# Optimization experiments

Measured on AMD Instinct MI355X. Metric: run time of the kernel, lower is better.

## Reference

```python
import jax, jax.numpy as jnp
import numpy as np

B_SZ = 64
SEQ = 2048
IN_DIM = 16
D_MODEL = 128
D_INNER = 256   # expand(2) * d_model
D_STATE = 16
N_LAYERS = 5
N_PARAMS = 3
IDX_PRICE, IDX_RY, IDX_GY, IDX_NY = 0, 1, 2, 3


def setup_inputs() -> dict:
    key = jax.random.key(0)
    ks = iter(jax.random.split(key, 64))
    def nrm(shape, scale=0.02):
        return jax.random.normal(next(ks), shape, jnp.float32) * scale
    inp = {}
    # forward args
    inp["origins"] = jax.random.uniform(next(ks), (B_SZ, SEQ, IN_DIM), jnp.float32, 0.5, 1.5)
    inp["x"] = jax.random.normal(next(ks), (B_SZ, SEQ, IN_DIM), jnp.float32)
    # input embedding
    inp["emb_w"] = nrm((IN_DIM, D_MODEL)); inp["emb_b"] = jnp.zeros((D_MODEL,), jnp.float32)
    # per-layer Mamba block params, stacked on leading n_layers dim
    inp["in_w"] = nrm((N_LAYERS, D_MODEL, 2 * D_INNER)); inp["in_b"] = jnp.zeros((N_LAYERS, 2 * D_INNER), jnp.float32)
    inp["xp_w"] = nrm((N_LAYERS, D_INNER, 2 * D_STATE)); inp["xp_b"] = jnp.zeros((N_LAYERS, 2 * D_STATE), jnp.float32)
    inp["dt_w"] = nrm((N_LAYERS, D_INNER, D_INNER));     inp["dt_b"] = jnp.zeros((N_LAYERS, D_INNER), jnp.float32)
    inp["out_w"] = nrm((N_LAYERS, D_INNER, D_MODEL));    inp["out_b"] = jnp.zeros((N_LAYERS, D_MODEL), jnp.float32)
    # A_log init: log(arange(1, d_state+1)) broadcast over d_inner
    a = jnp.log(jnp.arange(1, D_STATE + 1, dtype=jnp.float32))
    inp["A_log"] = jnp.broadcast_to(a, (N_LAYERS, D_INNER, D_STATE)).copy()
    inp["Dp"] = jnp.ones((N_LAYERS, D_INNER), jnp.float32)
    # layernorms
    inp["ln_g"] = jnp.ones((N_LAYERS, D_MODEL), jnp.float32)
    inp["ln_b"] = jnp.zeros((N_LAYERS, D_MODEL), jnp.float32)
    # output head: Linear(128,64) -> ReLU -> Linear(64,3) -> Sigmoid
    inp["o1_w"] = nrm((D_MODEL, D_MODEL // 2)); inp["o1_b"] = jnp.zeros((D_MODEL // 2,), jnp.float32)
    inp["o2_w"] = nrm((D_MODEL // 2, N_PARAMS)); inp["o2_b"] = jnp.zeros((N_PARAMS,), jnp.float32)
    return inp


def _silu(x):
    return x * jax.nn.sigmoid(x)


def _layernorm(x, g, b, eps=1e-5):
    mu = jnp.mean(x, axis=-1, keepdims=True)
    var = jnp.mean(jnp.square(x - mu), axis=-1, keepdims=True)
    return (x - mu) * jax.lax.rsqrt(var + eps) * g + b


def _mamba_block(x, iw, ib, xw, xb, dw, db, ow, ob, alog, d):
    # x: [B, S, D_MODEL]
    xz = x @ iw + ib                       # [B,S,2*di]
    x_proj, z = jnp.split(xz, 2, axis=-1)  # [B,S,di] each
    u = _silu(x_proj)                      # no conv path (use_conv=False)
    A = -jnp.exp(alog)                     # [di, ds]
    x_dbl = u @ xw + xb                    # [B,S,2*ds]
    Bm, Cm = jnp.split(x_dbl, 2, axis=-1)  # [B,S,ds]
    dt = jax.nn.softplus(u @ dw + db)      # [B,S,di]

    def step(h, t):
        u_t, dt_t, B_t, C_t = t            # [B,di],[B,di],[B,ds],[B,ds]
        dA = jnp.exp(dt_t[:, :, None] * A)                 # [B,di,ds]
        h = h * dA + (dt_t * u_t)[:, :, None] * B_t[:, None, :]
        y = jnp.sum(h * C_t[:, None, :], axis=-1) + d * u_t  # [B,di]
        return h, y

    h0 = jnp.zeros((u.shape[0], u.shape[2], A.shape[-1]), u.dtype)
    xs = (jnp.swapaxes(u, 0, 1), jnp.swapaxes(dt, 0, 1),
          jnp.swapaxes(Bm, 0, 1), jnp.swapaxes(Cm, 0, 1))  # seq-major
    _, ys = jax.lax.scan(step, h0, xs)     # ys: [S,B,di]
    y = jnp.swapaxes(ys, 0, 1)             # [B,S,di]
    y = y * _silu(z)
    return y @ ow + ob                     # [B,S,D_MODEL]


def _forward(origins, x, emb_w, emb_b, in_w, in_b, xp_w, xp_b, dt_w, dt_b,
             out_w, out_b, A_log, Dp, ln_g, ln_b, o1_w, o1_b, o2_w, o2_b):
    h = x @ emb_w + emb_b
    for l in range(N_LAYERS):
        res = h
        h = _mamba_block(h, in_w[l], in_b[l], xp_w[l], xp_b[l], dt_w[l], dt_b[l],
                         out_w[l], out_b[l], A_log[l], Dp[l])
        h = _layernorm(h + res, ln_g[l], ln_b[l])
    pooled = jnp.mean(h, axis=1)                         # lengths=None path
    hid = jax.nn.relu(pooled @ o1_w + o1_b)              # dropout is eval no-op
    params = jax.nn.sigmoid(hid @ o2_w + o2_b) * 2.0     # [B, 3]
    a, b, c = params[:, 0], params[:, 1], params[:, 2]
    last_1 = origins[:, -1, :]
    last_2 = origins[:, -2, :]
    price = last_1[:, IDX_PRICE]
    ry_now, ry_before = last_1[:, IDX_RY], last_2[:, IDX_RY]
    gy_now, gy_before = last_1[:, IDX_GY], last_2[:, IDX_GY]
    ny_now, ny_before = last_1[:, IDX_NY], last_2[:, IDX_NY]
    out = price * a * ry_now / ry_before * 2.0 * (
        b * jax.nn.sigmoid(gy_now - gy_before) + c * jax.nn.sigmoid(ny_now - ny_before))
    return out  # [B]


def reference(origins, x, emb_w, emb_b, in_w, in_b, xp_w, xp_b, dt_w, dt_b,
              out_w, out_b, A_log, Dp, ln_g, ln_b, o1_w, o1_b, o2_w, o2_b):
    return _forward(origins, x, emb_w, emb_b, in_w, in_b, xp_w, xp_b, dt_w, dt_b,
                    out_w, out_b, A_log, Dp, ln_g, ln_b, o1_w, o1_b, o2_w, o2_b)
```

## Files before the change

kernel.cpp:

```cpp
#include <hip/hip_runtime.h>
#include <hip/hip_bf16.h>
#include <math.h>

#define B_SZ    64
#define SEQ     2048
#define DMODEL  128
#define DINNER  256
#define DSTATE  16
#define NLAYERS 5
#define NSEG    32
#define LSEG    64

typedef unsigned short u16;
typedef __attribute__((ext_vector_type(8))) short bf16x8;
typedef __attribute__((ext_vector_type(4))) float f32x4;

static __device__ __forceinline__ float bf2f(u16 u){
  union { unsigned u; float f; } a; a.u = ((unsigned)u) << 16; return a.f;
}
static __device__ __forceinline__ u16 f2bf(float f){
  union { float f; unsigned u; } a; a.f = f;
  unsigned r = a.u + 0x7fffu + ((a.u >> 16) & 1u);
  return (u16)(r >> 16);
}
static __device__ __forceinline__ float sigm(float x){ return 1.f/(1.f+__expf(-x)); }
static __device__ __forceinline__ float siluf(float x){ return x/(1.f+__expf(-x)); }

#define MFMA16(a,b,c) __builtin_amdgcn_mfma_f32_16x16x32_bf16((a),(b),(c),0,0,0)

__global__ __launch_bounds__(256) void prep_kernel(
    const float* __restrict__ in_w, const float* __restrict__ xp_w,
    const float* __restrict__ dt_w, const float* __restrict__ out_w,
    u16* __restrict__ WT1, u16* __restrict__ WT2, u16* __restrict__ WT3){
  int idx = blockIdx.x*256 + threadIdx.x;
  const int n1 = NLAYERS*512*128, n2 = NLAYERS*288*256, n3 = NLAYERS*128*256;
  if (idx < n1){
    int l = idx/(512*128), r = idx%(512*128), n = r/128, k = r%128;
    WT1[idx] = f2bf(in_w[((size_t)l*128 + k)*512 + n]);
  } else if (idx < n1+n2){
    int t = idx-n1; int l=t/(288*256), r=t%(288*256), n=r/256, k=r%256;
    float v = (n<32) ? xp_w[((size_t)l*256+k)*32 + n]
                     : dt_w[((size_t)l*256+k)*256 + (n-32)];
    WT2[t] = f2bf(v);
  } else if (idx < n1+n2+n3){
    int t = idx-n1-n2; int l=t/(128*256), r=t%(128*256), n=r/256, k=r%256;
    WT3[t] = f2bf(out_w[((size_t)l*256+k)*128 + n]);
  }
}

__global__ __launch_bounds__(256) void emb_kernel(
    const float* __restrict__ x, const float* __restrict__ ew,
    const float* __restrict__ eb, u16* __restrict__ Hb, size_t cs){
  int idx = blockIdx.x*256 + threadIdx.x;
  int m = idx >> 7, d = idx & 127;
  float s = eb[d];
  #pragma unroll
  for (int k=0;k<16;++k) s += x[(size_t)m*16+k]*ew[k*128+d];
  Hb[(size_t)(d>>4)*cs + (size_t)m*16 + (d&15)] = f2bf(s);
}

__global__ __launch_bounds__(256) void gemm1_kernel(
    const u16* __restrict__ Hb, const u16* __restrict__ WT,
    const float* __restrict__ bias, u16* __restrict__ U, u16* __restrict__ ZS,
    size_t cs){
  const int lane = threadIdx.x & 63, wave = threadIdx.x >> 6;
  const int half = blockIdx.x & 1;
  const int m0 = (blockIdx.x >> 1)*256 + wave*64;
  const int lr = lane & 15, kg = lane >> 4;
  bf16x8 hfrag[4][4];
  #pragma unroll
  for (int g=0; g<4; ++g)
    #pragma unroll
    for (int f=0; f<4; ++f)
      hfrag[g][f] = *(const bf16x8*)(Hb + (size_t)((kg>>1)+2*f)*cs
                                     + (size_t)(m0+g*16+lr)*16 + (kg&1)*8);
  u16* const dst = half ? ZS : U;
  const u16* wrow = WT + (size_t)(half*256+lr)*128 + kg*8;
  bf16x8 wv[4];
  #pragma unroll
  for (int f=0; f<4; ++f) wv[f] = *(const bf16x8*)(wrow + f*32);
  #pragma unroll
  for (int nn=0; nn<16; ++nn){
    bf16x8 wn[4];
    if (nn < 15){
      const u16* wr2 = wrow + (size_t)(nn+1)*16*128;
      #pragma unroll
      for (int f=0; f<4; ++f) wn[f] = *(const bf16x8*)(wr2 + f*32);
    }
    f32x4 acc[4];
    #pragma unroll
    for (int g=0; g<4; ++g){
      acc[g] = (f32x4){0.f,0.f,0.f,0.f};
      #pragma unroll
      for (int f=0; f<4; ++f) acc[g] = MFMA16(wv[f], hfrag[g][f], acc[g]);
    }
    float4 bs4 = *(const float4*)(bias + half*256 + nn*16 + kg*4);
    #pragma unroll
    for (int g=0; g<4; ++g){
      ushort4 uv;
      uv.x = f2bf(siluf(acc[g][0]+bs4.x));
      uv.y = f2bf(siluf(acc[g][1]+bs4.y));
      uv.z = f2bf(siluf(acc[g][2]+bs4.z));
      uv.w = f2bf(siluf(acc[g][3]+bs4.w));
      *(ushort4*)(dst + (size_t)nn*cs + (size_t)(m0+g*16+lr)*16 + kg*4) = uv;
    }
    #pragma unroll
    for (int f=0; f<4; ++f) wv[f] = wn[f];
  }
}

__global__ __launch_bounds__(256) void gemm2_kernel(
    const u16* __restrict__ Uin, const u16* __restrict__ WT,
    const float* __restrict__ xpb, const float* __restrict__ dtb,
    u16* __restrict__ BC, u16* __restrict__ DT, size_t cs){
  const int lane = threadIdx.x & 63, wave = threadIdx.x >> 6;
  const int m0 = blockIdx.x*128 + wave*32;
  const int lr = lane & 15, kg = lane >> 6 ? 0 : (lane >> 4);
  const int kgr = lane >> 4;
  bf16x8 hfrag[2][8];
  #pragma unroll
  for (int g=0; g<2; ++g)
    #pragma unroll
    for (int f=0; f<8; ++f)
      hfrag[g][f] = *(const bf16x8*)(Uin + (size_t)((kgr>>1)+2*f)*cs
                                     + (size_t)(m0+g*16+lr)*16 + (kgr&1)*8);
  const u16* wrow = WT + (size_t)lr*256 + kgr*8;
  bf16x8 wv[8];
  #pragma unroll
  for (int f=0; f<8; ++f) wv[f] = *(const bf16x8*)(wrow + f*32);
  #pragma unroll
  for (int nn=0; nn<18; ++nn){
    bf16x8 wn[8];
    if (nn < 17){
      const u16* wr2 = wrow + (size_t)(nn+1)*16*256;
      #pragma unroll
      for (int f=0; f<8; ++f) wn[f] = *(const bf16x8*)(wr2 + f*32);
    }
    f32x4 acc[2];
    #pragma unroll
    for (int g=0; g<2; ++g){
      acc[g] = (f32x4){0.f,0.f,0.f,0.f};
      #pragma unroll
      for (int f=0; f<8; ++f) acc[g] = MFMA16(wv[f], hfrag[g][f], acc[g]);
    }
    const int col0 = nn*16 + kgr*4;
    if (col0 < 32){
      float4 bs4 = *(const float4*)(xpb + col0);
      #pragma unroll
      for (int g=0; g<2; ++g){
        ushort4 uv;
        uv.x = f2bf(acc[g][0]+bs4.x); uv.y = f2bf(acc[g][1]+bs4.y);
        uv.z = f2bf(acc[g][2]+bs4.z); uv.w = f2bf(acc[g][3]+bs4.w);
        *(ushort4*)(BC + (size_t)nn*cs + (size_t)(m0+g*16+lr)*16 + kgr*4) = uv;
      }
    } else {
      float4 bs4 = *(const float4*)(dtb + (col0-32));
      #pragma unroll
      for (int g=0; g<2; ++g){
        float v0=acc[g][0]+bs4.x, v1=acc[g][1]+bs4.y;
        float v2=acc[g][2]+bs4.z, v3=acc[g][3]+bs4.w;
        ushort4 uv;
        uv.x = f2bf(fmaxf(v0,0.f) + __logf(1.f + __expf(-fabsf(v0))));
        uv.y = f2bf(fmaxf(v1,0.f) + __logf(1.f + __expf(-fabsf(v1))));
        uv.z = f2bf(fmaxf(v2,0.f) + __logf(1.f + __expf(-fabsf(v2))));
        uv.w = f2bf(fmaxf(v3,0.f) + __logf(1.f + __expf(-fabsf(v3))));
        *(ushort4*)(DT + (size_t)(nn-2)*cs + (size_t)(m0+g*16+lr)*16 + kgr*4) = uv;
      }
    }
    #pragma unroll
    for (int f=0; f<8; ++f) wv[f] = wn[f];
  }
}

static __device__ __forceinline__ void powtree(float r, float* pw){
  float p2=r*r, p3=p2*r, p4=p2*p2;
  float p5=p4*r, p6=p4*p2, p7=p4*p3, p8=p4*p4;
  pw[0]=r;  pw[1]=p2; pw[2]=p3; pw[3]=p4;
  pw[4]=p5; pw[5]=p6; pw[6]=p7; pw[7]=p8;
  pw[8]=p8*r;  pw[9]=p8*p2;  pw[10]=p8*p3;  pw[11]=p8*p4;
  pw[12]=p8*p5; pw[13]=p8*p6; pw[14]=p8*p7; pw[15]=p8*p8;
}

__global__ __launch_bounds__(256) void scan_p1(
    const u16* __restrict__ U, const u16* __restrict__ DT,
    const u16* __restrict__ BC, const float* __restrict__ Alog,
    u16* __restrict__ SGH, float* __restrict__ SDT, size_t cs){
  const int seg = blockIdx.x % NSEG;
  const int b   = blockIdx.x / NSEG;
  const int c   = threadIdx.x;
  const size_t coff = (size_t)(c>>4)*cs + (c&15);
  float a2[16]; bool geo = true;
  #pragma unroll
  for (int i=0;i<16;++i){
    float A = -__expf(Alog[c*16+i]);
    a2[i] = A * 1.44269504f;
    if (fabsf(A + (float)(i+1)) > 1e-3f) geo = false;
  }
  float h[16];
  #pragma unroll
  for (int i=0;i<16;++i) h[i]=0.f;
  float sdt = 0.f;
  const size_t mbase = (size_t)b*SEQ + (size_t)seg*LSEG;
  if (geo){
    for (int t=0;t<LSEG;++t){
      const size_t m = mbase + t;
      float u  = bf2f(U [coff + m*16]);
      float dt = bf2f(DT[coff + m*16]);
      bf16x8 b0 = *(const bf16x8*)(BC + m*16);
      bf16x8 b1 = *(const bf16x8*)(BC + m*16 + 8);
      float du = dt*u; sdt += dt;
      float r = exp2f(-1.44269504f*dt);
      float pw[16]; powtree(r, pw);
      #pragma unroll
      for (int i=0;i<8;++i)  h[i]   = h[i]  *pw[i]   + du*bf2f((u16)b0[i]);
      #pragma unroll
      for (int i=8;i<16;++i) h[i]   = h[i]  *pw[i]   + du*bf2f((u16)b1[i-8]);
    }
  } else {
    for (int t=0;t<LSEG;++t){
      const size_t m = mbase + t;
      float u  = bf2f(U [coff + m*16]);
      float dt = bf2f(DT[coff + m*16]);
      bf16x8 b0 = *(const bf16x8*)(BC + m*16);
      bf16x8 b1 = *(const bf16x8*)(BC + m*16 + 8);
      float du = dt*u; sdt += dt;
      #pragma unroll
      for (int i=0;i<16;++i){
        float Bv = (i<8) ? bf2f((u16)b0[i]) : bf2f((u16)b1[i-8]);
        h[i] = h[i]*exp2f(dt*a2[i]) + du*Bv;
      }
    }
  }
  const size_t kb = ((size_t)b*NSEG+seg);
  #pragma unroll
  for (int i=0;i<16;++i) SGH[(kb*16+i)*256 + c] = f2bf(h[i]);
  SDT[kb*256 + c] = sdt;
}

__global__ __launch_bounds__(256) void scan_p2(
    u16* __restrict__ SGH, const float* __restrict__ SDT,
    const float* __restrict__ Alog){
  const int i = blockIdx.x & 15, b = blockIdx.x >> 4, c = threadIdx.x;
  const float a2 = -__expf(Alog[c*16+i]) * 1.44269504f;
  float h = 0.f;
  for (int s=0;s<NSEG;++s){
    const size_t kb = ((size_t)b*NSEG+s);
    float sdt = SDT[kb*256 + c];
    size_t k = (kb*16+i)*256 + c;
    float hl = bf2f(SGH[k]);
    SGH[k] = f2bf(h);
    h = h*exp2f(sdt*a2) + hl;
  }
}

__global__ __launch_bounds__(256) void scan3ln_kernel(
    const u16* __restrict__ U, const u16* __restrict__ DT,
    const u16* __restrict__ BC, const u16* __restrict__ ZS,
    const float* __restrict__ Alog, const float* __restrict__ Dp,
    const u16* __restrict__ SGH, const u16* __restrict__ WT,
    const float* __restrict__ ob, const float* __restrict__ gv,
    const float* __restrict__ bbv, u16* __restrict__ Hb, size_t cs){
  __shared__ u16 ysl[LSEG*264];
  const int seg = blockIdx.x % NSEG;
  const int b   = blockIdx.x / NSEG;
  {
    const int c = threadIdx.x;
    const size_t coff = (size_t)(c>>4)*cs + (c&15);
    float a2[16]; bool geo = true;
    #pragma unroll
    for (int i=0;i<16;++i){
      float A = -__expf(Alog[c*16+i]);
      a2[i] = A * 1.44269504f;
      if (fabsf(A + (float)(i+1)) > 1e-3f) geo = false;
    }
    const float Dv = Dp[c];
    const size_t kb = ((size_t)b*NSEG+seg);
    float h[16];
    #pragma unroll
    for (int i=0;i<16;++i) h[i] = bf2f(SGH[(kb*16+i)*256 + c]);
    const size_t mbase = (size_t)b*SEQ + (size_t)seg*LSEG;
    if (geo){
      for (int t=0;t<LSEG;++t){
        const size_t m = mbase + t;
        float u  = bf2f(U [coff + m*16]);
        float dt = bf2f(DT[coff + m*16]);
        float zs = bf2f(ZS[coff + m*16]);
        bf16x8 b0 = *(const bf16x8*)(BC + m*16);
        bf16x8 b1 = *(const bf16x8*)(BC + m*16 + 8);
        bf16x8 c0 = *(const bf16x8*)(BC + cs + m*16);
        bf16x8 c1 = *(const bf16x8*)(BC + cs + m*16 + 8);
        float du = dt*u;
        float r = exp2f(-1.44269504f*dt);
        float pw[16]; powtree(r, pw);
        float s0=0.f, s1=0.f;
        #pragma unroll
        for (int i=0;i<8;++i){
          h[i] = h[i]*pw[i] + du*bf2f((u16)b0[i]);
          s0 += h[i]*bf2f((u16)c0[i]);
        }
        #pragma unroll
        for (int i=8;i<16;++i){
          h[i] = h[i]*pw[i] + du*bf2f((u16)b1[i-8]);
          s1 += h[i]*bf2f((u16)c1[i-8]);
        }
        float y = s0 + s1 + Dv*u;
        ysl[t*264 + c] = f2bf(y*zs);
      }
    } else {
      for (int t=0;t<LSEG;++t){
        const size_t m = mbase + t;
        float u  = bf2f(U [coff + m*16]);
        float dt = bf2f(DT[coff + m*16]);
        float zs = bf2f(ZS[coff + m*16]);
        bf16x8 b0 = *(const bf16x8*)(BC + m*16);
        bf16x8 b1 = *(const bf16x8*)(BC + m*16 + 8);
        bf16x8 c0 = *(const bf16x8*)(BC + cs + m*16);
        bf16x8 c1 = *(const bf16x8*)(BC + cs + m*16 + 8);
        float du = dt*u;
        float s0=0.f, s1=0.f;
        #pragma unroll
        for (int i=0;i<8;++i){
          h[i] = h[i]*exp2f(dt*a2[i]) + du*bf2f((u16)b0[i]);
          s0 += h[i]*bf2f((u16)c0[i]);
        }
        #pragma unroll
        for (int i=8;i<16;++i){
          h[i] = h[i]*exp2f(dt*a2[i]) + du*bf2f((u16)b1[i-8]);
          s1 += h[i]*bf2f((u16)c1[i-8]);
        }
        float y = s0 + s1 + Dv*u;
        ysl[t*264 + c] = f2bf(y*zs);
      }
    }
  }
  __syncthreads();
  {
    const int lane = threadIdx.x & 63, wave = threadIdx.x >> 6;
    const int lr = lane & 15, kg = lane >> 4;
    const int lw = wave*16 + lr;
    const size_t m = (size_t)b*SEQ + (size_t)seg*LSEG + lw;
    bf16x8 hfrag[8];
    #pragma unroll
    for (int f=0; f<8; ++f)
      hfrag[f] = *(const bf16x8*)(&ysl[lw*264 + kg*8 + f*32]);
    const u16* wrow = WT + (size_t)lr*256 + kg*8;
    bf16x8 wv[8];
    #pragma unroll
    for (int f=0; f<8; ++f) wv[f] = *(const bf16x8*)(wrow + f*32);
    ushort4 xvp[8];
    float s = 0.f, q = 0.f;
    #pragma unroll
    for (int n=0; n<8; ++n){
      bf16x8 wn[8];
      if (n < 7){
        const u16* wr2 = wrow + (size_t)(n+1)*16*256;
        #pragma unroll
        for (int f=0; f<8; ++f) wn[f] = *(const bf16x8*)(wr2 + f*32);
      }
      f32x4 acc = {0.f,0.f,0.f,0.f};
      #pragma unroll
      for (int f=0; f<8; ++f) acc = MFMA16(wv[f], hfrag[f], acc);
      const int col0 = n*16 + kg*4;
      float4 bs4 = *(const float4*)(ob + col0);
      ushort4 rs = *(const ushort4*)(Hb + (size_t)n*cs + m*16 + kg*4);
      float x0 = acc[0] + bs4.x + bf2f(rs.x);
      float x1 = acc[1] + bs4.y + bf2f(rs.y);
      float x2 = acc[2] + bs4.z + bf2f(rs.z);
      float x3 = acc[3] + bs4.w + bf2f(rs.w);
      s += (x0+x1)+(x2+x3);
      q += (x0*x0+x1*x1)+(x2*x2+x3*x3);
      ushort4 pv; pv.x=f2bf(x0); pv.y=f2bf(x1); pv.z=f2bf(x2); pv.w=f2bf(x3);
      xvp[n] = pv;
      #pragma unroll
      for (int f=0; f<8; ++f) wv[f] = wn[f];
    }
    s += __shfl_xor(s,16); q += __shfl_xor(q,16);
    s += __shfl_xor(s,32); q += __shfl_xor(q,32);
    float mu  = s * 0.0078125f;
    float var = q * 0.0078125f - mu*mu;
    float inv = rsqrtf(var + 1e-5f);
    #pragma unroll
    for (int n=0;n<8;++n){
      const int col0 = n*16 + kg*4;
      float4 g4 = *(const float4*)(gv  + col0);
      float4 b4 = *(const float4*)(bbv + col0);
      ushort4 pv = xvp[n];
      ushort4 uv;
      uv.x = f2bf((bf2f(pv.x)-mu)*inv*g4.x + b4.x);
      uv.y = f2bf((bf2f(pv.y)-mu)*inv*g4.y + b4.y);
      uv.z = f2bf((bf2f(pv.z)-mu)*inv*g4.z + b4.z);
      uv.w = f2bf((bf2f(pv.w)-mu)*inv*g4.w + b4.w);
      *(ushort4*)(Hb + (size_t)n*cs + m*16 + kg*4) = uv;
    }
  }
}

__global__ __launch_bounds__(128) void pool1_kernel(
    const u16* __restrict__ Hb, float* __restrict__ PP, size_t cs){
  const int blk = blockIdx.x;
  const int tc = blk & 15, b = blk >> 4;
  const int d = threadIdx.x;
  const size_t coff = (size_t)(d>>4)*cs + (d&15);
  float s = 0.f;
  const size_t base = ((size_t)b*SEQ + tc*128);
  for (int t=0;t<128;++t) s += bf2f(Hb[coff + (base+t)*16]);
  PP[((size_t)b*16 + tc)*128 + d] = s;
}
__global__ __launch_bounds__(128) void pool2_kernel(
    const float* __restrict__ PP, float* __restrict__ P){
  const int b = blockIdx.x, d = threadIdx.x;
  float s = 0.f;
  #pragma unroll
  for (int tc=0;tc<16;++tc) s += PP[((size_t)b*16+tc)*128 + d];
  P[b*128 + d] = s * (1.f/SEQ);
}

__global__ __launch_bounds__(64) void head_kernel(
    const float* __restrict__ P, const float* __restrict__ o1w,
    const float* __restrict__ o1b, const float* __restrict__ o2w,
    const float* __restrict__ o2b, const float* __restrict__ origins,
    float* __restrict__ out){
  const int b = blockIdx.x;
  const int j = threadIdx.x;
  float hv = o1b[j];
  #pragma unroll 4
  for (int d=0; d<128; ++d) hv += P[b*128+d]*o1w[d*64+j];
  hv = fmaxf(hv, 0.f);
  float p0 = hv*o2w[j*3+0], p1 = hv*o2w[j*3+1], p2 = hv*o2w[j*3+2];
  #pragma unroll
  for (int o=1;o<64;o<<=1){
    p0 += __shfl_xor(p0,o); p1 += __shfl_xor(p1,o); p2 += __shfl_xor(p2,o);
  }
  if (j == 0){
    float a = 2.f*sigm(p0 + o2b[0]);
    float bb = 2.f*sigm(p1 + o2b[1]);
    float c = 2.f*sigm(p2 + o2b[2]);
    const float* l1 = origins + ((size_t)b*SEQ + (SEQ-1))*16;
    const float* l2 = origins + ((size_t)b*SEQ + (SEQ-2))*16;
    float price=l1[0], ry_n=l1[1], ry_b=l2[1], gy_n=l1[2], gy_b=l2[2], ny_n=l1[3], ny_b=l2[3];
    out[b] = price*a*ry_n/ry_b*2.f*(bb*sigm(gy_n-gy_b) + c*sigm(ny_n-ny_b));
  }
}

extern "C" void kernel_launch(void* const* d_in, const int* in_sizes, int n_in,
                              void* d_out, int out_size, void* d_ws, size_t ws_size,
                              hipStream_t stream){
  const float* origins = (const float*)d_in[0];
  const float* x      = (const float*)d_in[1];
  const float* emb_w  = (const float*)d_in[2];
  const float* emb_b  = (const float*)d_in[3];
  const float* in_w   = (const float*)d_in[4];
  const float* in_b   = (const float*)d_in[5];
  const float* xp_w   = (const float*)d_in[6];
  const float* xp_b   = (const float*)d_in[7];
  const float* dt_w   = (const float*)d_in[8];
  const float* dt_b   = (const float*)d_in[9];
  const float* out_w  = (const float*)d_in[10];
  const float* out_b  = (const float*)d_in[11];
  const float* A_log  = (const float*)d_in[12];
  const float* Dp     = (const float*)d_in[13];
  const float* ln_g   = (const float*)d_in[14];
  const float* ln_b   = (const float*)d_in[15];
  const float* o1_w   = (const float*)d_in[16];
  const float* o1_b   = (const float*)d_in[17];
  const float* o2_w   = (const float*)d_in[18];
  const float* o2_b   = (const float*)d_in[19];
  float* outp = (float*)d_out;

  auto al = [](size_t b)->size_t{ return (b + 255) & ~(size_t)255; };
  const size_t wt1_b = al((size_t)NLAYERS*512*128*2);
  const size_t wt2_b = al((size_t)NLAYERS*288*256*2);
  const size_t wt3_b = al((size_t)NLAYERS*128*256*2);
  const size_t po_b  = al((size_t)B_SZ*128*4);
  const size_t pp_b  = al((size_t)B_SZ*16*128*4);
  const size_t fixed = wt1_b + wt2_b + wt3_b + po_b + pp_b;

  int CB = 0;
  static const int cbc[7] = {64,32,16,8,4,2,1};
  size_t hb_b=0, u_b=0, bc_b=0, sgh_b=0, sdt_b=0;
  for (int i=0;i<7;++i){
    int cb = cbc[i];
    size_t csz = (size_t)cb*SEQ*16;
    size_t hbb = al(8*csz*2);
    size_t uu  = al(16*csz*2);
    size_t bb  = al(2*csz*2);
    size_t sgh = al((size_t)cb*NSEG*DSTATE*DINNER*2);
    size_t sdt = al((size_t)cb*NSEG*DINNER*4);
    if (fixed + hbb + 3*uu + bb + sgh + sdt <= ws_size){
      CB=cb; hb_b=hbb; u_b=uu; bc_b=bb; sgh_b=sgh; sdt_b=sdt; break;
    }
  }
  if (!CB) return;

  char* ws = (char*)d_ws;
  size_t off = 0;
  auto take = [&](size_t bytes)->char*{ char* p = ws + off; off += bytes; return p; };
  u16*   WT1 = (u16*)take(wt1_b);
  u16*   WT2 = (u16*)take(wt2_b);
  u16*   WT3 = (u16*)take(wt3_b);
  float* PO  = (float*)take(po_b);
  float* PP  = (float*)take(pp_b);
  u16*   Hb  = (u16*)take(hb_b);
  u16*   U   = (u16*)take(u_b);
  u16*   ZS  = (u16*)take(u_b);
  u16*   DT  = (u16*)take(u_b);
  u16*   BC  = (u16*)take(bc_b);
  u16*   SGH = (u16*)take(sgh_b);
  float* SDT = (float*)take(sdt_b);

  prep_kernel<<<3360, 256, 0, stream>>>(in_w, xp_w, dt_w, out_w, WT1, WT2, WT3);

  const int NC = B_SZ / CB;
  const int Mc = CB * SEQ;
  const size_t cs = (size_t)Mc*16;
  for (int ci=0; ci<NC; ++ci){
    const int b0 = ci * CB;
    const size_t R0 = (size_t)b0 * SEQ;
    emb_kernel<<<(Mc*DMODEL)/256, 256, 0, stream>>>(x + R0*16, emb_w, emb_b, Hb, cs);
    for (int l=0;l<NLAYERS;++l){
      const float* Al = A_log + (size_t)l*DINNER*DSTATE;
      gemm1_kernel<<<(Mc/256)*2, 256, 0, stream>>>(Hb, WT1 + (size_t)l*512*128,
                                                   in_b + l*512, U, ZS, cs);
      gemm2_kernel<<<Mc/128, 256, 0, stream>>>(U, WT2 + (size_t)l*288*256,
                                               xp_b + l*32, dt_b + l*256, BC, DT, cs);
      scan_p1<<<CB*NSEG, 256, 0, stream>>>(U, DT, BC, Al, SGH, SDT, cs);
      scan_p2<<<CB*16, 256, 0, stream>>>(SGH, SDT, Al);
      scan3ln_kernel<<<CB*NSEG, 256, 0, stream>>>(U, DT, BC, ZS, Al, Dp + l*DINNER,
                                                  SGH, WT3 + (size_t)l*128*256,
                                                  out_b + l*128, ln_g + l*128,
                                                  ln_b + l*128, Hb, cs);
    }
    pool1_kernel<<<CB*16, 128, 0, stream>>>(Hb, PP, cs);
    pool2_kernel<<<CB, 128, 0, stream>>>(PP, PO + (size_t)b0*128);
  }
  head_kernel<<<B_SZ, 64, 0, stream>>>(PO, o1_w, o1_b, o2_w, o2_b, origins, outp);
}
```

Measured before the change: 1.955 ms.

## Split fused scan+out-proj kernel into scan pass and separate GEMM+LayerNorm kernel

The fused scan3ln kernel, which ran the selective scan into shared memory and then the output projection with layernorm, is split in two. scan_p3 runs the scan and writes the gated output in place over U in the chunked global layout. A new gemm3ln_kernel then does the out-projection, residual add and layernorm, with each wave handling 32 rows over two fragment groups so every weight load is reused twice. This drops the shared-memory staging and lets each kernel have its own occupancy, but adds a global write and re-read of the scan output plus an extra launch per layer. A small cleanup in gemm2 removes a redundant lane-index variable.

```diff
diff --git a/kernel.cpp b/kernel.cpp
--- a/kernel.cpp
+++ b/kernel.cpp
@@ -115,16 +115,15 @@
     u16* __restrict__ BC, u16* __restrict__ DT, size_t cs){
   const int lane = threadIdx.x & 63, wave = threadIdx.x >> 6;
   const int m0 = blockIdx.x*128 + wave*32;
-  const int lr = lane & 15, kg = lane >> 6 ? 0 : (lane >> 4);
-  const int kgr = lane >> 4;
+  const int lr = lane & 15, kg = lane >> 4;
   bf16x8 hfrag[2][8];
   #pragma unroll
   for (int g=0; g<2; ++g)
     #pragma unroll
     for (int f=0; f<8; ++f)
-      hfrag[g][f] = *(const bf16x8*)(Uin + (size_t)((kgr>>1)+2*f)*cs
-                                     + (size_t)(m0+g*16+lr)*16 + (kgr&1)*8);
-  const u16* wrow = WT + (size_t)lr*256 + kgr*8;
+      hfrag[g][f] = *(const bf16x8*)(Uin + (size_t)((kg>>1)+2*f)*cs
+                                     + (size_t)(m0+g*16+lr)*16 + (kg&1)*8);
+  const u16* wrow = WT + (size_t)lr*256 + kg*8;
   bf16x8 wv[8];
   #pragma unroll
   for (int f=0; f<8; ++f) wv[f] = *(const bf16x8*)(wrow + f*32);
@@ -143,7 +142,7 @@
       #pragma unroll
       for (int f=0; f<8; ++f) acc[g] = MFMA16(wv[f], hfrag[g][f], acc[g]);
     }
-    const int col0 = nn*16 + kgr*4;
+    const int col0 = nn*16 + kg*4;
     if (col0 < 32){
       float4 bs4 = *(const float4*)(xpb + col0);
       #pragma unroll
@@ -151,7 +150,7 @@
         ushort4 uv;
         uv.x = f2bf(acc[g][0]+bs4.x); uv.y = f2bf(acc[g][1]+bs4.y);
         uv.z = f2bf(acc[g][2]+bs4.z); uv.w = f2bf(acc[g][3]+bs4.w);
-        *(ushort4*)(BC + (size_t)nn*cs + (size_t)(m0+g*16+lr)*16 + kgr*4) = uv;
+        *(ushort4*)(BC + (size_t)nn*cs + (size_t)(m0+g*16+lr)*16 + kg*4) = uv;
       }
     } else {
       float4 bs4 = *(const float4*)(dtb + (col0-32));
@@ -164,7 +163,7 @@
         uv.y = f2bf(fmaxf(v1,0.f) + __logf(1.f + __expf(-fabsf(v1))));
         uv.z = f2bf(fmaxf(v2,0.f) + __logf(1.f + __expf(-fabsf(v2))));
         uv.w = f2bf(fmaxf(v3,0.f) + __logf(1.f + __expf(-fabsf(v3))));
-        *(ushort4*)(DT + (size_t)(nn-2)*cs + (size_t)(m0+g*16+lr)*16 + kgr*4) = uv;
+        *(ushort4*)(DT + (size_t)(nn-2)*cs + (size_t)(m0+g*16+lr)*16 + kg*4) = uv;
       }
     }
     #pragma unroll
@@ -253,138 +252,144 @@
   }
 }
 
-__global__ __launch_bounds__(256) void scan3ln_kernel(
-    const u16* __restrict__ U, const u16* __restrict__ DT,
-    const u16* __restrict__ BC, const u16* __restrict__ ZS,
-    const float* __restrict__ Alog, const float* __restrict__ Dp,
-    const u16* __restrict__ SGH, const u16* __restrict__ WT,
-    const float* __restrict__ ob, const float* __restrict__ gv,
-    const float* __restrict__ bbv, u16* __restrict__ Hb, size_t cs){
-  __shared__ u16 ysl[LSEG*264];
+__global__ __launch_bounds__(256) void scan_p3(
+    u16* __restrict__ UY, const u16* __restrict__ DT, const u16* __restrict__ BC,
+    const u16* __restrict__ ZS, const float* __restrict__ Alog,
+    const float* __restrict__ Dp, const u16* __restrict__ SGH, size_t cs){
   const int seg = blockIdx.x % NSEG;
   const int b   = blockIdx.x / NSEG;
-  {
-    const int c = threadIdx.x;
-    const size_t coff = (size_t)(c>>4)*cs + (c&15);
-    float a2[16]; bool geo = true;
-    #pragma unroll
-    for (int i=0;i<16;++i){
-      float A = -__expf(Alog[c*16+i]);
-      a2[i] = A * 1.44269504f;
-      if (fabsf(A + (float)(i+1)) > 1e-3f) geo = false;
-    }
-    const float Dv = Dp[c];
-    const size_t kb = ((size_t)b*NSEG+seg);
-    float h[16];
-    #pragma unroll
-    for (int i=0;i<16;++i) h[i] = bf2f(SGH[(kb*16+i)*256 + c]);
-    const size_t mbase = (size_t)b*SEQ + (size_t)seg*LSEG;
-    if (geo){
-      for (int t=0;t<LSEG;++t){
-        const size_t m = mbase + t;
-        float u  = bf2f(U [coff + m*16]);
-        float dt = bf2f(DT[coff + m*16]);
-        float zs = bf2f(ZS[coff + m*16]);
-        bf16x8 b0 = *(const bf16x8*)(BC + m*16);
-        bf16x8 b1 = *(const bf16x8*)(BC + m*16 + 8);
-        bf16x8 c0 = *(const bf16x8*)(BC + cs + m*16);
-        bf16x8 c1 = *(const bf16x8*)(BC + cs + m*16 + 8);
-        float du = dt*u;
-        float r = exp2f(-1.44269504f*dt);
-        float pw[16]; powtree(r, pw);
-        float s0=0.f, s1=0.f;
-        #pragma unroll
-        for (int i=0;i<8;++i){
-          h[i] = h[i]*pw[i] + du*bf2f((u16)b0[i]);
-          s0 += h[i]*bf2f((u16)c0[i]);
-        }
-        #pragma unroll
-        for (int i=8;i<16;++i){
-          h[i] = h[i]*pw[i] + du*bf2f((u16)b1[i-8]);
-          s1 += h[i]*bf2f((u16)c1[i-8]);
-        }
-        float y = s0 + s1 + Dv*u;
-        ysl[t*264 + c] = f2bf(y*zs);
-      }
-    } else {
-      for (int t=0;t<LSEG;++t){
-        const size_t m = mbase + t;
-        float u  = bf2f(U [coff + m*16]);
-        float dt = bf2f(DT[coff + m*16]);
-        float zs = bf2f(ZS[coff + m*16]);
-        bf16x8 b0 = *(const bf16x8*)(BC + m*16);
-        bf16x8 b1 = *(const bf16x8*)(BC + m*16 + 8);
-        bf16x8 c0 = *(const bf16x8*)(BC + cs + m*16);
-        bf16x8 c1 = *(const bf16x8*)(BC + cs + m*16 + 8);
-        float du = dt*u;
-        float s0=0.f, s1=0.f;
-        #pragma unroll
-        for (int i=0;i<8;++i){
-          h[i] = h[i]*exp2f(dt*a2[i]) + du*bf2f((u16)b0[i]);
-          s0 += h[i]*bf2f((u16)c0[i]);
-        }
-        #pragma unroll
-        for (int i=8;i<16;++i){
-          h[i] = h[i]*exp2f(dt*a2[i]) + du*bf2f((u16)b1[i-8]);
-          s1 += h[i]*bf2f((u16)c1[i-8]);
-        }
-        float y = s0 + s1 + Dv*u;
-        ysl[t*264 + c] = f2bf(y*zs);
-      }
-    }
-  }
-  __syncthreads();
-  {
-    const int lane = threadIdx.x & 63, wave = threadIdx.x >> 6;
-    const int lr = lane & 15, kg = lane >> 4;
-    const int lw = wave*16 + lr;
-    const size_t m = (size_t)b*SEQ + (size_t)seg*LSEG + lw;
-    bf16x8 hfrag[8];
+  const int c   = threadIdx.x;
+  const size_t coff = (size_t)(c>>4)*cs + (c&15);
+  float a2[16]; bool geo = true;
+  #pragma unroll
+  for (int i=0;i<16;++i){
+    float A = -__expf(Alog[c*16+i]);
+    a2[i] = A * 1.44269504f;
+    if (fabsf(A + (float)(i+1)) > 1e-3f) geo = false;
+  }
+  const float Dv = Dp[c];
+  const size_t kb = ((size_t)b*NSEG+seg);
+  float h[16];
+  #pragma unroll
+  for (int i=0;i<16;++i) h[i] = bf2f(SGH[(kb*16+i)*256 + c]);
+  const size_t mbase = (size_t)b*SEQ + (size_t)seg*LSEG;
+  if (geo){
+    for (int t=0;t<LSEG;++t){
+      const size_t m = mbase + t;
+      float u  = bf2f(UY[coff + m*16]);
+      float dt = bf2f(DT[coff + m*16]);
+      float zs = bf2f(ZS[coff + m*16]);
+      bf16x8 b0 = *(const bf16x8*)(BC + m*16);
+      bf16x8 b1 = *(const bf16x8*)(BC + m*16 + 8);
+      bf16x8 c0 = *(const bf16x8*)(BC + cs + m*16);
+      bf16x8 c1 = *(const bf16x8*)(BC + cs + m*16 + 8);
+      float du = dt*u;
+      float r = exp2f(-1.44269504f*dt);
+      float pw[16]; powtree(r, pw);
+      float s0=0.f, s1=0.f;
+      #pragma unroll
+      for (int i=0;i<8;++i){
+        h[i] = h[i]*pw[i] + du*bf2f((u16)b0[i]);
+        s0 += h[i]*bf2f((u16)c0[i]);
+      }
+      #pragma unroll
+      for (int i=8;i<16;++i){
+        h[i] = h[i]*pw[i] + du*bf2f((u16)b1[i-8]);
+        s1 += h[i]*bf2f((u16)c1[i-8]);
+      }
+      float y = s0 + s1 + Dv*u;
+      UY[coff + m*16] = f2bf(y*zs);
+    }
+  } else {
+    for (int t=0;t<LSEG;++t){
+      const size_t m = mbase + t;
+      float u  = bf2f(UY[coff + m*16]);
+      float dt = bf2f(DT[coff + m*16]);
+      float zs = bf2f(ZS[coff + m*16]);
+      bf16x8 b0 = *(const bf16x8*)(BC + m*16);
+      bf16x8 b1 = *(const bf16x8*)(BC + m*16 + 8);
+      bf16x8 c0 = *(const bf16x8*)(BC + cs + m*16);
+      bf16x8 c1 = *(const bf16x8*)(BC + cs + m*16 + 8);
+      float du = dt*u;
+      float s0=0.f, s1=0.f;
+      #pragma unroll
+      for (int i=0;i<8;++i){
+        h[i] = h[i]*exp2f(dt*a2[i]) + du*bf2f((u16)b0[i]);
+        s0 += h[i]*bf2f((u16)c0[i]);
+      }
+      #pragma unroll
+      for (int i=8;i<16;++i){
+        h[i] = h[i]*exp2f(dt*a2[i]) + du*bf2f((u16)b1[i-8]);
+        s1 += h[i]*bf2f((u16)c1[i-8]);
+      }
+      float y = s0 + s1 + Dv*u;
+      UY[coff + m*16] = f2bf(y*zs);
+    }
+  }
+}
+
+__global__ __launch_bounds__(256) void gemm3ln_kernel(
+    const u16* __restrict__ YS, const u16* __restrict__ WT,
+    const float* __restrict__ ob, const float* __restrict__ g,
+    const float* __restrict__ bb, u16* __restrict__ Hb, size_t cs){
+  const int lane = threadIdx.x & 63, wave = threadIdx.x >> 6;
+  const int m0 = blockIdx.x*128 + wave*32;
+  const int lr = lane & 15, kg = lane >> 4;
+  bf16x8 hfrag[2][8];
+  #pragma unroll
+  for (int gg=0; gg<2; ++gg)
     #pragma unroll
     for (int f=0; f<8; ++f)
-      hfrag[f] = *(const bf16x8*)(&ysl[lw*264 + kg*8 + f*32]);
-    const u16* wrow = WT + (size_t)lr*256 + kg*8;
-    bf16x8 wv[8];
-    #pragma unroll
-    for (int f=0; f<8; ++f) wv[f] = *(const bf16x8*)(wrow + f*32);
-    ushort4 xvp[8];
-    float s = 0.f, q = 0.f;
-    #pragma unroll
-    for (int n=0; n<8; ++n){
-      bf16x8 wn[8];
-      if (n < 7){
-        const u16* wr2 = wrow + (size_t)(n+1)*16*256;
-        #pragma unroll
-        for (int f=0; f<8; ++f) wn[f] = *(const bf16x8*)(wr2 + f*32);
-      }
+      hfrag[gg][f] = *(const bf16x8*)(YS + (size_t)((kg>>1)+2*f)*cs
+                                      + (size_t)(m0+gg*16+lr)*16 + (kg&1)*8);
+  const u16* wrow = WT + (size_t)lr*256 + kg*8;
+  bf16x8 wv[8];
+  #pragma unroll
+  for (int f=0; f<8; ++f) wv[f] = *(const bf16x8*)(wrow + f*32);
+  ushort4 xvp[2][8];
+  float s[2] = {0.f,0.f}, q[2] = {0.f,0.f};
+  #pragma unroll
+  for (int n=0; n<8; ++n){
+    bf16x8 wn[8];
+    if (n < 7){
+      const u16* wr2 = wrow + (size_t)(n+1)*16*256;
+      #pragma unroll
+      for (int f=0; f<8; ++f) wn[f] = *(const bf16x8*)(wr2 + f*32);
+    }
+    float4 bs4 = *(const float4*)(ob + n*16 + kg*4);
+    #pragma unroll
+    for (int gg=0; gg<2; ++gg){
       f32x4 acc = {0.f,0.f,0.f,0.f};
       #pragma unroll
-      for (int f=0; f<8; ++f) acc = MFMA16(wv[f], hfrag[f], acc);
-      const int col0 = n*16 + kg*4;
-      float4 bs4 = *(const float4*)(ob + col0);
+      for (int f=0; f<8; ++f) acc = MFMA16(wv[f], hfrag[gg][f], acc);
+      const size_t m = (size_t)(m0 + gg*16 + lr);
       ushort4 rs = *(const ushort4*)(Hb + (size_t)n*cs + m*16 + kg*4);
       float x0 = acc[0] + bs4.x + bf2f(rs.x);
       float x1 = acc[1] + bs4.y + bf2f(rs.y);
       float x2 = acc[2] + bs4.z + bf2f(rs.z);
       float x3 = acc[3] + bs4.w + bf2f(rs.w);
-      s += (x0+x1)+(x2+x3);
-      q += (x0*x0+x1*x1)+(x2*x2+x3*x3);
+      s[gg] += (x0+x1)+(x2+x3);
+      q[gg] += (x0*x0+x1*x1)+(x2*x2+x3*x3);
       ushort4 pv; pv.x=f2bf(x0); pv.y=f2bf(x1); pv.z=f2bf(x2); pv.w=f2bf(x3);
-      xvp[n] = pv;
-      #pragma unroll
-      for (int f=0; f<8; ++f) wv[f] = wn[f];
-    }
-    s += __shfl_xor(s,16); q += __shfl_xor(q,16);
-    s += __shfl_xor(s,32); q += __shfl_xor(q,32);
-    float mu  = s * 0.0078125f;
-    float var = q * 0.0078125f - mu*mu;
+      xvp[gg][n] = pv;
+    }
+    #pragma unroll
+    for (int f=0; f<8; ++f) wv[f] = wn[f];
+  }
+  #pragma unroll
+  for (int gg=0; gg<2; ++gg){
+    float ss = s[gg], qq = q[gg];
+    ss += __shfl_xor(ss,16); qq += __shfl_xor(qq,16);
+    ss += __shfl_xor(ss,32); qq += __shfl_xor(qq,32);
+    float mu  = ss * 0.0078125f;
+    float var = qq * 0.0078125f - mu*mu;
     float inv = rsqrtf(var + 1e-5f);
+    const size_t m = (size_t)(m0 + gg*16 + lr);
     #pragma unroll
     for (int n=0;n<8;++n){
-      const int col0 = n*16 + kg*4;
-      float4 g4 = *(const float4*)(gv  + col0);
-      float4 b4 = *(const float4*)(bbv + col0);
-      ushort4 pv = xvp[n];
+      float4 g4 = *(const float4*)(g  + n*16 + kg*4);
+      float4 b4 = *(const float4*)(bb + n*16 + kg*4);
+      ushort4 pv = xvp[gg][n];
       ushort4 uv;
       uv.x = f2bf((bf2f(pv.x)-mu)*inv*g4.x + b4.x);
       uv.y = f2bf((bf2f(pv.y)-mu)*inv*g4.y + b4.y);
@@ -525,10 +530,11 @@
                                                xp_b + l*32, dt_b + l*256, BC, DT, cs);
       scan_p1<<<CB*NSEG, 256, 0, stream>>>(U, DT, BC, Al, SGH, SDT, cs);
       scan_p2<<<CB*16, 256, 0, stream>>>(SGH, SDT, Al);
-      scan3ln_kernel<<<CB*NSEG, 256, 0, stream>>>(U, DT, BC, ZS, Al, Dp + l*DINNER,
-                                                  SGH, WT3 + (size_t)l*128*256,
-                                                  out_b + l*128, ln_g + l*128,
-                                                  ln_b + l*128, Hb, cs);
+      scan_p3<<<CB*NSEG, 256, 0, stream>>>(U, DT, BC, ZS, Al, Dp + l*DINNER,
+                                           SGH, cs);
+      gemm3ln_kernel<<<Mc/128, 256, 0, stream>>>(U, WT3 + (size_t)l*128*256,
+                                                 out_b + l*128, ln_g + l*128,
+                                                 ln_b + l*128, Hb, cs);
     }
     pool1_kernel<<<CB*16, 128, 0, stream>>>(Hb, PP, cs);
     pool2_kernel<<<CB, 128, 0, stream>>>(PP, PO + (size_t)b0*128);
```

Result: faster. 1.829 ms, median of 2 (-6.4%).
